# Kernel optimization log

Hardware: AMD Instinct MI355X
Metric: run time of the kernel (lower is better)

Reference implementation:

```python
import jax, jax.numpy as jnp
import numpy as np

N, C_S, C_Z, H, D = 512, 384, 128, 16, 24  # c_hidden per head
EPS = 1e-5

def _ln(x, g, b):
    m = jnp.mean(x, axis=-1, keepdims=True)
    v = jnp.mean(jnp.square(x - m), axis=-1, keepdims=True)
    return (x - m) * jax.lax.rsqrt(v + EPS) * g + b

def setup_inputs() -> dict:
    key = jax.random.key(0)
    ks = jax.random.split(key, 12)
    s = lambda fan: 1.0 / np.sqrt(fan)
    return {
        "a": jax.random.normal(ks[0], (1, N, C_S), jnp.float32),
        "z": jax.random.normal(ks[1], (1, N, N, C_Z), jnp.float32),
        "g_a": jnp.ones((C_S,), jnp.float32),
        "b_a": jnp.zeros((C_S,), jnp.float32),
        "g_z": jnp.ones((C_Z,), jnp.float32),
        "b_z": jnp.zeros((C_Z,), jnp.float32),
        "Wz": jax.random.normal(ks[2], (C_Z, H), jnp.float32) * s(C_Z),
        "bz": jnp.zeros((H,), jnp.float32),
        "Wq": jax.random.normal(ks[3], (C_S, H * D), jnp.float32) * s(C_S),
        "Wk": jax.random.normal(ks[4], (C_S, H * D), jnp.float32) * s(C_S),
        "Wv": jax.random.normal(ks[5], (C_S, H * D), jnp.float32) * s(C_S),
        "Wg": jax.random.normal(ks[6], (C_S, H * D), jnp.float32) * s(C_S),
        "bg": jnp.zeros((H * D,), jnp.float32),
        "Wo": jax.random.normal(ks[7], (H * D, C_S), jnp.float32) * s(H * D),
        "bo": jnp.zeros((C_S,), jnp.float32),
    }

def reference(a, z, g_a, b_a, g_z, b_z, Wz, bz, Wq, Wk, Wv, Wg, bg, Wo, bo):
    B = a.shape[0]
    a_n = _ln(a, g_a, b_a)                       # [B,N,C_S]
    z_n = _ln(z, g_z, b_z)                       # [B,N,N,C_Z]
    # linear_z then permute(0,3,1,2): [B,N,N,H] -> [B,H,N,N]
    pair_bias = jnp.einsum('bijc,ch->bhij', z_n, Wz) + bz[None, :, None, None]
    q = (a_n @ Wq).reshape(B, N, H, D) * (1.0 / np.sqrt(D))
    k = (a_n @ Wk).reshape(B, N, H, D)
    v = (a_n @ Wv).reshape(B, N, H, D)
    scores = jnp.einsum('bqhd,bkhd->bhqk', q, k) + pair_bias
    p = jax.nn.softmax(scores, axis=-1)
    o = jnp.einsum('bhqk,bkhd->bqhd', p, v)      # [B,N,H,D]
    g = jax.nn.sigmoid(a_n @ Wg + bg).reshape(B, N, H, D)
    o = (o * g).reshape(B, N, H * D)
    return o @ Wo + bo                            # [B,N,C_S]
```

## Files before the change

### kernel.cpp

```cpp
#include <hip/hip_runtime.h>
#include <math.h>

#define N 512
#define CS 384
#define CZ 128
#define NH 16
#define DH 24
#define HD 384
#define NN (N*N)
#define EPS 1e-5f

#define OFF_AN   0
#define OFF_QT   196608
#define OFF_KT   393216
#define OFF_VT   589824
#define OFF_GT   786432
#define OFF_OG   983040
#define OFF_WZ2  1179648
#define OFF_SH   1181696
#define OFF_BH   1181712
#define OFF_BIAS 1181728

__global__ void __launch_bounds__(256) ln_prep_kernel(const float* __restrict__ a, const float* __restrict__ g_a,
                                                      const float* __restrict__ b_a, float* __restrict__ an_out,
                                                      const float* __restrict__ g_z, const float* __restrict__ lnb_z,
                                                      const float* __restrict__ Wz, const float* __restrict__ bz,
                                                      float* __restrict__ wz2, float* __restrict__ sh,
                                                      float* __restrict__ bh) {
    __shared__ float ls[NH][17], lb[NH][17];
    __shared__ float l1[4], l2[4];
    const int t = threadIdx.x;
    if (blockIdx.x == 256) {
        for (int i = t; i < NH * CZ; i += 256) {
            int h = i >> 7, c = i & (CZ - 1);
            wz2[h * CZ + c] = g_z[c] * Wz[c * NH + h];
        }
        int h = t >> 4, seg = t & 15;
        float s = 0.f, b = 0.f;
        #pragma unroll
        for (int i = 0; i < 8; ++i) {
            int c = seg * 8 + i;
            float w = Wz[c * NH + h];
            s += g_z[c] * w;
            b += lnb_z[c] * w;
        }
        ls[h][seg] = s; lb[h][seg] = b;
        __syncthreads();
        if (t < NH) {
            float ss = 0.f, bb = 0.f;
            #pragma unroll
            for (int i = 0; i < 16; ++i) { ss += ls[t][i]; bb += lb[t][i]; }
            sh[t] = ss;
            bh[t] = bb + bz[t];
        }
        return;
    }
    const int half = t >> 7;
    const int tr = t & 127;
    const int r = blockIdx.x * 2 + half;
    const float* row = a + r * CS;
    float x0 = row[tr], x1 = row[tr + 128], x2 = row[tr + 256];
    float s1 = x0 + x1 + x2;
    float s2 = x0 * x0 + x1 * x1 + x2 * x2;
    #pragma unroll
    for (int m = 1; m < 64; m <<= 1) {
        s1 += __shfl_xor(s1, m, 64);
        s2 += __shfl_xor(s2, m, 64);
    }
    if ((t & 63) == 0) { l1[t >> 6] = s1; l2[t >> 6] = s2; }
    __syncthreads();
    s1 = l1[half * 2] + l1[half * 2 + 1];
    s2 = l2[half * 2] + l2[half * 2 + 1];
    float mu = s1 * (1.f / CS);
    float var = s2 * (1.f / CS) - mu * mu;
    float rs = rsqrtf(var + EPS);
    float* an = an_out + r * CS;
    an[tr]       = (x0 - mu) * rs * g_a[tr]       + b_a[tr];
    an[tr + 128] = (x1 - mu) * rs * g_a[tr + 128] + b_a[tr + 128];
    an[tr + 256] = (x2 - mu) * rs * g_a[tr + 256] + b_a[tr + 256];
}

__global__ void __launch_bounds__(256) qkvg_kernel(const float* __restrict__ Wq, const float* __restrict__ Wk,
                                                   const float* __restrict__ Wv, const float* __restrict__ Wg,
                                                   const float* __restrict__ bg, const float* __restrict__ an,
                                                   float* __restrict__ qt, float* __restrict__ kt,
                                                   float* __restrict__ vt, float* __restrict__ gt) {
    __shared__ float4 lan[64 * 8];
    const int t = threadIdx.x;
    const int lane = t & 63;
    const int w = __builtin_amdgcn_readfirstlane(t >> 6);
    const int s = blockIdx.x * 4 + w;
    const int n0 = s * 4;
    const int sel = n0 / HD;
    const int col = n0 - sel * HD;
    const float* Wm = (sel == 0) ? Wq : (sel == 1) ? Wk : (sel == 2) ? Wv : Wg;
    const int m0 = blockIdx.y * 64;
    const int m = m0 + lane;
    const float4* an4 = (const float4*)an;
    float acc[4];
    #pragma unroll
    for (int j = 0; j < 4; ++j) acc[j] = 0.f;
    for (int kb = 0; kb < CS; kb += 32) {
        __syncthreads();
        #pragma unroll
        for (int i = 0; i < 2; ++i) {
            const int idx = i * 256 + t;
            const int r = idx >> 3, c = idx & 7;
            lan[(r << 3) + (c ^ (r & 7))] = an4[(size_t)(m0 + r) * 96 + (kb >> 2) + c];
        }
        __syncthreads();
        float4 av[8];
        #pragma unroll
        for (int i = 0; i < 8; ++i) av[i] = lan[(lane << 3) + (i ^ (lane & 7))];
        #pragma unroll
        for (int i = 0; i < 8; ++i) {
            const float* wr = Wm + (kb + i * 4) * HD + col;
            #pragma unroll
            for (int j = 0; j < 4; ++j) {
                acc[j] += av[i].x * wr[j];
                acc[j] += av[i].y * wr[HD + j];
                acc[j] += av[i].z * wr[2 * HD + j];
                acc[j] += av[i].w * wr[3 * HD + j];
            }
        }
    }
    float* dst = (sel == 0) ? qt : (sel == 1) ? kt : (sel == 2) ? vt : gt;
    if (sel == 3) {
        #pragma unroll
        for (int j = 0; j < 4; ++j) acc[j] = 1.f / (1.f + __expf(-(acc[j] + bg[col + j])));
    } else if (sel == 0) {
        #pragma unroll
        for (int j = 0; j < 4; ++j) acc[j] *= 0.20412414523193153f;
    }
    const int h = col / DH, d0 = col - h * DH;
    float* dp = dst + (h * N + m) * DH + d0;
    #pragma unroll
    for (int j = 0; j < 4; ++j) dp[j] = acc[j];
}

__global__ void __launch_bounds__(256, 4) pairbias_kernel(const float* __restrict__ z,
                                                          const float* __restrict__ wz2,
                                                          const float* __restrict__ sh,
                                                          const float* __restrict__ bh,
                                                          float* __restrict__ bias) {
    __shared__ float4 lz[64 * 32];
    const int t = threadIdx.x;
    const int l = t & 63;
    const int w = __builtin_amdgcn_readfirstlane(t >> 6);
    const int h0 = w * 4;
    const int row0 = blockIdx.x * 64;

    const float4* zsrc = (const float4*)(z + (size_t)row0 * CZ);
    #pragma unroll
    for (int i = 0; i < 8; ++i) {
        const int g4 = i * 256 + t;
        float4 v = zsrc[g4];
        const int r = g4 >> 5, cc = g4 & 31;
        lz[r * 32 + (cc ^ (r & 31))] = v;
    }
    __syncthreads();

    const unsigned base = (unsigned)(l * 512 + ((l & 31) << 4));
    const char* lzb = (const char*)lz;
    float s1 = 0.f, s2 = 0.f;
    float dots[4];
    #pragma unroll
    for (int j = 0; j < 4; ++j) dots[j] = 0.f;
    #pragma unroll
    for (int cc = 0; cc < 32; ++cc) {
        float4 v = *(const float4*)(lzb + (base ^ (unsigned)(cc << 4)));
        s1 += v.x + v.y + v.z + v.w;
        s2 += v.x * v.x + v.y * v.y + v.z * v.z + v.w * v.w;
        #pragma unroll
        for (int j = 0; j < 4; ++j) {
            const float4 wv = ((const float4*)(wz2 + (h0 + j) * CZ))[cc];
            dots[j] += v.x * wv.x + v.y * wv.y + v.z * wv.z + v.w * wv.w;
        }
    }
    const float mu = s1 * (1.f / CZ);
    const float var = s2 * (1.f / CZ) - mu * mu;
    const float rr = rsqrtf(var + EPS);
    const int row = row0 + l;
    #pragma unroll
    for (int j = 0; j < 4; ++j)
        bias[(h0 + j) * NN + row] = rr * (dots[j] - mu * sh[h0 + j]) + bh[h0 + j];
}

__global__ void __launch_bounds__(256, 4) attn_kernel(const float* __restrict__ qt, const float* __restrict__ kt,
                                                      const float* __restrict__ vt, const float* __restrict__ gt,
                                                      const float* __restrict__ bias, float* __restrict__ og) {
    __shared__ float4 lzK[128 * 8];
    __shared__ float4 lzV[128 * 8];
    const int t = threadIdx.x;
    const int lane = t & 63;
    const int w = __builtin_amdgcn_readfirstlane(t >> 6);
    const int qhalf = lane >> 5;
    const int klane = lane & 31;
    const int h = blockIdx.y;
    const int q = blockIdx.x * 8 + w * 2 + qhalf;
    const float* qT = qt + h * N * DH;
    const float4* kT4 = (const float4*)(kt + h * N * DH);
    const float4* vT4 = (const float4*)(vt + h * N * DH);
    const float* brow = bias + h * NN + q * N;

    float qv[DH];
    #pragma unroll
    for (int d6 = 0; d6 < 6; ++d6) {
        float4 t4 = ((const float4*)(qT + q * DH))[d6];
        qv[d6 * 4 + 0] = t4.x; qv[d6 * 4 + 1] = t4.y; qv[d6 * 4 + 2] = t4.z; qv[d6 * 4 + 3] = t4.w;
    }
    float m_run = -1e30f, l_run = 0.f;
    float acc[DH];
    #pragma unroll
    for (int d = 0; d < DH; ++d) acc[d] = 0.f;

    for (int tile = 0; tile < 4; ++tile) {
        __syncthreads();
        const int kt0 = tile * 128;
        #pragma unroll
        for (int i = 0; i < 3; ++i) {
            const int idx = i * 256 + t;
            const int r = idx / 6, c = idx - r * 6;
            const int slot = (r << 3) + (c ^ (r & 7));
            lzK[slot] = kT4[kt0 * 6 + idx];
            lzV[slot] = vT4[kt0 * 6 + idx];
        }
        __syncthreads();
        float sc[4];
        #pragma unroll
        for (int j = 0; j < 4; ++j) {
            const int kk = j * 32 + klane;
            const float4* kr = lzK + (kk << 3);
            const int x = kk & 7;
            float4 k0 = kr[0 ^ x], k1 = kr[1 ^ x], k2 = kr[2 ^ x],
                   k3 = kr[3 ^ x], k4 = kr[4 ^ x], k5 = kr[5 ^ x];
            float s = qv[0]*k0.x + qv[1]*k0.y + qv[2]*k0.z + qv[3]*k0.w
                    + qv[4]*k1.x + qv[5]*k1.y + qv[6]*k1.z + qv[7]*k1.w
                    + qv[8]*k2.x + qv[9]*k2.y + qv[10]*k2.z + qv[11]*k2.w
                    + qv[12]*k3.x + qv[13]*k3.y + qv[14]*k3.z + qv[15]*k3.w
                    + qv[16]*k4.x + qv[17]*k4.y + qv[18]*k4.z + qv[19]*k4.w
                    + qv[20]*k5.x + qv[21]*k5.y + qv[22]*k5.z + qv[23]*k5.w;
            sc[j] = s + brow[kt0 + kk];
        }
        float tm = fmaxf(fmaxf(sc[0], sc[1]), fmaxf(sc[2], sc[3]));
        #pragma unroll
        for (int m = 1; m < 32; m <<= 1) tm = fmaxf(tm, __shfl_xor(tm, m, 64));
        const float m_new = fmaxf(m_run, tm);
        const float scale = __expf(m_run - m_new);
        l_run *= scale;
        #pragma unroll
        for (int d = 0; d < DH; ++d) acc[d] *= scale;
        float p[4], ps = 0.f;
        #pragma unroll
        for (int j = 0; j < 4; ++j) { p[j] = __expf(sc[j] - m_new); ps += p[j]; }
        #pragma unroll
        for (int m = 1; m < 32; m <<= 1) ps += __shfl_xor(ps, m, 64);
        l_run += ps;
        m_run = m_new;
        #pragma unroll
        for (int j = 0; j < 4; ++j) {
            const int kk = j * 32 + klane;
            const float4* vr = lzV + (kk << 3);
            const int x = kk & 7;
            float4 v0 = vr[0 ^ x], v1 = vr[1 ^ x], v2 = vr[2 ^ x],
                   v3 = vr[3 ^ x], v4 = vr[4 ^ x], v5 = vr[5 ^ x];
            const float pj = p[j];
            acc[0] += pj*v0.x;  acc[1] += pj*v0.y;  acc[2] += pj*v0.z;  acc[3] += pj*v0.w;
            acc[4] += pj*v1.x;  acc[5] += pj*v1.y;  acc[6] += pj*v1.z;  acc[7] += pj*v1.w;
            acc[8] += pj*v2.x;  acc[9] += pj*v2.y;  acc[10] += pj*v2.z; acc[11] += pj*v2.w;
            acc[12] += pj*v3.x; acc[13] += pj*v3.y; acc[14] += pj*v3.z; acc[15] += pj*v3.w;
            acc[16] += pj*v4.x; acc[17] += pj*v4.y; acc[18] += pj*v4.z; acc[19] += pj*v4.w;
            acc[20] += pj*v5.x; acc[21] += pj*v5.y; acc[22] += pj*v5.z; acc[23] += pj*v5.w;
        }
    }
    #pragma unroll
    for (int m = 1; m < 32; m <<= 1) {
        #pragma unroll
        for (int d = 0; d < DH; ++d) acc[d] += __shfl_xor(acc[d], m, 64);
    }
    const float inv = 1.f / l_run;
    float o = 0.f;
    #pragma unroll
    for (int d = 0; d < DH; ++d) o = (klane == d) ? acc[d] : o;
    if (klane < DH) {
        float g = gt[h * N * DH + q * DH + klane];
        og[q * HD + h * DH + klane] = o * inv * g;
    }
}

__global__ void __launch_bounds__(256) out_gemm_kernel(const float* __restrict__ Wo, const float* __restrict__ bo,
                                                       const float* __restrict__ og, float* __restrict__ out) {
    __shared__ float4 lo[64 * 8];
    const int t = threadIdx.x;
    const int lane = t & 63;
    const int w = __builtin_amdgcn_readfirstlane(t >> 6);
    const int s = blockIdx.x * 4 + w;
    const int c0 = s * 2;
    const int m0 = blockIdx.y * 64;
    const int m = m0 + lane;
    const float4* og4 = (const float4*)og;
    float acc[2];
    acc[0] = 0.f; acc[1] = 0.f;
    for (int kb = 0; kb < HD; kb += 32) {
        __syncthreads();
        #pragma unroll
        for (int i = 0; i < 2; ++i) {
            const int idx = i * 256 + t;
            const int r = idx >> 3, c = idx & 7;
            lo[(r << 3) + (c ^ (r & 7))] = og4[(size_t)(m0 + r) * 96 + (kb >> 2) + c];
        }
        __syncthreads();
        float4 av[8];
        #pragma unroll
        for (int i = 0; i < 8; ++i) av[i] = lo[(lane << 3) + (i ^ (lane & 7))];
        #pragma unroll
        for (int i = 0; i < 8; ++i) {
            const float* wr = Wo + (kb + i * 4) * CS + c0;
            #pragma unroll
            for (int j = 0; j < 2; ++j) {
                acc[j] += av[i].x * wr[j];
                acc[j] += av[i].y * wr[CS + j];
                acc[j] += av[i].z * wr[2 * CS + j];
                acc[j] += av[i].w * wr[3 * CS + j];
            }
        }
    }
    #pragma unroll
    for (int j = 0; j < 2; ++j) out[m * CS + c0 + j] = acc[j] + bo[c0 + j];
}

extern "C" void kernel_launch(void* const* d_in, const int* in_sizes, int n_in,
                              void* d_out, int out_size, void* d_ws, size_t ws_size,
                              hipStream_t stream) {
    const float* a    = (const float*)d_in[0];
    const float* z    = (const float*)d_in[1];
    const float* g_a  = (const float*)d_in[2];
    const float* b_a  = (const float*)d_in[3];
    const float* g_z  = (const float*)d_in[4];
    const float* b_z  = (const float*)d_in[5];
    const float* Wz   = (const float*)d_in[6];
    const float* bz   = (const float*)d_in[7];
    const float* Wq   = (const float*)d_in[8];
    const float* Wk   = (const float*)d_in[9];
    const float* Wv   = (const float*)d_in[10];
    const float* Wg   = (const float*)d_in[11];
    const float* bg   = (const float*)d_in[12];
    const float* Wo   = (const float*)d_in[13];
    const float* bo   = (const float*)d_in[14];
    float* ws  = (float*)d_ws;
    float* out = (float*)d_out;

    float* an   = ws + OFF_AN;
    float* qt   = ws + OFF_QT;
    float* kt   = ws + OFF_KT;
    float* vt   = ws + OFF_VT;
    float* gt   = ws + OFF_GT;
    float* ogp  = ws + OFF_OG;
    float* wz2  = ws + OFF_WZ2;
    float* shp  = ws + OFF_SH;
    float* bhp  = ws + OFF_BH;
    float* bias = ws + OFF_BIAS;

    hipLaunchKernelGGL(ln_prep_kernel, dim3(257),    dim3(256), 0, stream,
                       a, g_a, b_a, an, g_z, b_z, Wz, bz, wz2, shp, bhp);
    hipLaunchKernelGGL(qkvg_kernel,    dim3(96, 8),  dim3(256), 0, stream,
                       Wq, Wk, Wv, Wg, bg, an, qt, kt, vt, gt);
    hipLaunchKernelGGL(pairbias_kernel, dim3(4096),  dim3(256), 0, stream,
                       z, wz2, shp, bhp, bias);
    hipLaunchKernelGGL(attn_kernel,    dim3(64, 16), dim3(256), 0, stream,
                       qt, kt, vt, gt, bias, ogp);
    hipLaunchKernelGGL(out_gemm_kernel, dim3(48, 8), dim3(256), 0, stream,
                       Wo, bo, ogp, out);
}
```

Measured before the change: 333.8 us.

## Double-buffer z tiles in pair-bias kernel with register prefetch across four slices

Each pair-bias block now handles 256 rows in four 64-row slices instead of one. The next slice's z data is prefetched into registers while the current slice is computed from shared memory, using two LDS buffers. The goal is to hide global-load latency behind the LayerNorm and projection math on this memory-bound kernel. The cost is four times fewer blocks, double the LDS, more registers and lower occupancy (launch bounds drop from 4 to 2).

```diff
diff --git a/kernel.cpp b/kernel.cpp
--- a/kernel.cpp
+++ b/kernel.cpp
@@ -138,52 +138,67 @@
     for (int j = 0; j < 4; ++j) dp[j] = acc[j];
 }
 
-__global__ void __launch_bounds__(256, 4) pairbias_kernel(const float* __restrict__ z,
+__global__ void __launch_bounds__(256, 2) pairbias_kernel(const float* __restrict__ z,
                                                           const float* __restrict__ wz2,
                                                           const float* __restrict__ sh,
                                                           const float* __restrict__ bh,
                                                           float* __restrict__ bias) {
-    __shared__ float4 lz[64 * 32];
+    __shared__ float4 buf0[64 * 32];
+    __shared__ float4 buf1[64 * 32];
     const int t = threadIdx.x;
     const int l = t & 63;
     const int w = __builtin_amdgcn_readfirstlane(t >> 6);
     const int h0 = w * 4;
-    const int row0 = blockIdx.x * 64;
-
-    const float4* zsrc = (const float4*)(z + (size_t)row0 * CZ);
-    #pragma unroll
-    for (int i = 0; i < 8; ++i) {
-        const int g4 = i * 256 + t;
-        float4 v = zsrc[g4];
-        const int r = g4 >> 5, cc = g4 & 31;
-        lz[r * 32 + (cc ^ (r & 31))] = v;
-    }
-    __syncthreads();
-
-    const unsigned base = (unsigned)(l * 512 + ((l & 31) << 4));
-    const char* lzb = (const char*)lz;
-    float s1 = 0.f, s2 = 0.f;
-    float dots[4];
-    #pragma unroll
-    for (int j = 0; j < 4; ++j) dots[j] = 0.f;
-    #pragma unroll
-    for (int cc = 0; cc < 32; ++cc) {
-        float4 v = *(const float4*)(lzb + (base ^ (unsigned)(cc << 4)));
-        s1 += v.x + v.y + v.z + v.w;
-        s2 += v.x * v.x + v.y * v.y + v.z * v.z + v.w * v.w;
-        #pragma unroll
-        for (int j = 0; j < 4; ++j) {
-            const float4 wv = ((const float4*)(wz2 + (h0 + j) * CZ))[cc];
-            dots[j] += v.x * wv.x + v.y * wv.y + v.z * wv.z + v.w * wv.w;
-        }
-    }
-    const float mu = s1 * (1.f / CZ);
-    const float var = s2 * (1.f / CZ) - mu * mu;
-    const float rr = rsqrtf(var + EPS);
-    const int row = row0 + l;
-    #pragma unroll
-    for (int j = 0; j < 4; ++j)
-        bias[(h0 + j) * NN + row] = rr * (dots[j] - mu * sh[h0 + j]) + bh[h0 + j];
+    const int row0 = blockIdx.x * 256;
+    const float4* zsrc = (const float4*)z + (size_t)row0 * 32;
+
+#define PB_LOAD(s, rr) { const float4* p_ = zsrc + (s) * 2048; \
+    _Pragma("unroll") for (int i = 0; i < 8; ++i) rr[i] = p_[i * 256 + t]; }
+
+#define PB_WRITE(rr, bufp) { _Pragma("unroll") for (int i = 0; i < 8; ++i) { \
+    const int g4_ = i * 256 + t; const int r_ = g4_ >> 5, cc_ = g4_ & 31; \
+    bufp[r_ * 32 + (cc_ ^ (r_ & 31))] = rr[i]; } }
+
+#define PB_COMPUTE(s, bufp) { \
+    const char* lzb_ = (const char*)bufp; \
+    const unsigned base_ = (unsigned)(l * 512 + ((l & 31) << 4)); \
+    float s1_ = 0.f, s2_ = 0.f, d0_ = 0.f, d1_ = 0.f, d2_ = 0.f, d3_ = 0.f; \
+    _Pragma("unroll") for (int cc = 0; cc < 32; ++cc) { \
+        float4 v_ = *(const float4*)(lzb_ + (base_ ^ (unsigned)(cc << 4))); \
+        s1_ += v_.x + v_.y + v_.z + v_.w; \
+        s2_ += v_.x * v_.x + v_.y * v_.y + v_.z * v_.z + v_.w * v_.w; \
+        const float4 w0_ = ((const float4*)(wz2 + (h0 + 0) * CZ))[cc]; \
+        const float4 w1_ = ((const float4*)(wz2 + (h0 + 1) * CZ))[cc]; \
+        const float4 w2_ = ((const float4*)(wz2 + (h0 + 2) * CZ))[cc]; \
+        const float4 w3_ = ((const float4*)(wz2 + (h0 + 3) * CZ))[cc]; \
+        d0_ += v_.x * w0_.x + v_.y * w0_.y + v_.z * w0_.z + v_.w * w0_.w; \
+        d1_ += v_.x * w1_.x + v_.y * w1_.y + v_.z * w1_.z + v_.w * w1_.w; \
+        d2_ += v_.x * w2_.x + v_.y * w2_.y + v_.z * w2_.z + v_.w * w2_.w; \
+        d3_ += v_.x * w3_.x + v_.y * w3_.y + v_.z * w3_.z + v_.w * w3_.w; } \
+    const float mu_ = s1_ * (1.f / CZ); \
+    const float var_ = s2_ * (1.f / CZ) - mu_ * mu_; \
+    const float rs_ = rsqrtf(var_ + EPS); \
+    const int row_ = row0 + (s) * 64 + l; \
+    bias[(h0 + 0) * NN + row_] = rs_ * (d0_ - mu_ * sh[h0 + 0]) + bh[h0 + 0]; \
+    bias[(h0 + 1) * NN + row_] = rs_ * (d1_ - mu_ * sh[h0 + 1]) + bh[h0 + 1]; \
+    bias[(h0 + 2) * NN + row_] = rs_ * (d2_ - mu_ * sh[h0 + 2]) + bh[h0 + 2]; \
+    bias[(h0 + 3) * NN + row_] = rs_ * (d3_ - mu_ * sh[h0 + 3]) + bh[h0 + 3]; }
+
+    float4 ra[8], rb[8];
+    PB_LOAD(0, ra); PB_WRITE(ra, buf0); __syncthreads();
+    PB_LOAD(1, rb);
+    PB_COMPUTE(0, buf0);
+    PB_WRITE(rb, buf1); __syncthreads();
+    PB_LOAD(2, ra);
+    PB_COMPUTE(1, buf1);
+    PB_WRITE(ra, buf0); __syncthreads();
+    PB_LOAD(3, rb);
+    PB_COMPUTE(2, buf0);
+    PB_WRITE(rb, buf1); __syncthreads();
+    PB_COMPUTE(3, buf1);
+#undef PB_LOAD
+#undef PB_WRITE
+#undef PB_COMPUTE
 }
 
 __global__ void __launch_bounds__(256, 4) attn_kernel(const float* __restrict__ qt, const float* __restrict__ kt,
@@ -365,7 +380,7 @@
                        a, g_a, b_a, an, g_z, b_z, Wz, bz, wz2, shp, bhp);
     hipLaunchKernelGGL(qkvg_kernel,    dim3(96, 8),  dim3(256), 0, stream,
                        Wq, Wk, Wv, Wg, bg, an, qt, kt, vt, gt);
-    hipLaunchKernelGGL(pairbias_kernel, dim3(4096),  dim3(256), 0, stream,
+    hipLaunchKernelGGL(pairbias_kernel, dim3(1024),  dim3(256), 0, stream,
                        z, wz2, shp, bhp, bias);
     hipLaunchKernelGGL(attn_kernel,    dim3(64, 16), dim3(256), 0, stream,
                        qt, kt, vt, gt, bias, ogp);
```

Result: slower. 399.5 us (+19.7%).

## Restructure pair-bias kernel so each thread owns a z row and computes all heads

Applied to the files above, without the earlier changes.

In the pair-bias kernel each block now stages 256 rows of z (128 KB of LDS) instead of 64. Each thread handles one row across all 16 heads, rather than one wave per 4 heads re-reading the same row. This removes the 4x redundant LDS reads and layernorm statistics per row. Global loads are issued as two register batches to overlap fetching with LDS writes. The trade-off is much higher LDS and register use, which limits the kernel to one block per CU and reduces latency hiding for the memory-bound z stream.

```diff
diff --git a/kernel.cpp b/kernel.cpp
--- a/kernel.cpp
+++ b/kernel.cpp
@@ -138,52 +138,61 @@
     for (int j = 0; j < 4; ++j) dp[j] = acc[j];
 }
 
-__global__ void __launch_bounds__(256, 4) pairbias_kernel(const float* __restrict__ z,
+__global__ void __launch_bounds__(256, 1) pairbias_kernel(const float* __restrict__ z,
                                                           const float* __restrict__ wz2,
                                                           const float* __restrict__ sh,
                                                           const float* __restrict__ bh,
                                                           float* __restrict__ bias) {
-    __shared__ float4 lz[64 * 32];
-    const int t = threadIdx.x;
-    const int l = t & 63;
-    const int w = __builtin_amdgcn_readfirstlane(t >> 6);
-    const int h0 = w * 4;
-    const int row0 = blockIdx.x * 64;
-
-    const float4* zsrc = (const float4*)(z + (size_t)row0 * CZ);
-    #pragma unroll
-    for (int i = 0; i < 8; ++i) {
-        const int g4 = i * 256 + t;
-        float4 v = zsrc[g4];
-        const int r = g4 >> 5, cc = g4 & 31;
-        lz[r * 32 + (cc ^ (r & 31))] = v;
-    }
+    __shared__ float4 lz[256 * 32];
+    const int t = threadIdx.x;
+    const int row0 = blockIdx.x * 256;
+    const float4* zsrc = (const float4*)z + (size_t)row0 * 32;
+
+#define PB_WR(rr, b) { _Pragma("unroll") for (int i = 0; i < 8; ++i) { \
+    const int g4_ = ((b) * 8 + i) * 256 + t; \
+    const int r_ = g4_ >> 5, cc_ = g4_ & 31; \
+    lz[r_ * 32 + (cc_ ^ (r_ & 31))] = rr[i]; } }
+
+    float4 ra[8], rb[8];
+    #pragma unroll
+    for (int i = 0; i < 8; ++i) ra[i] = zsrc[(0 * 8 + i) * 256 + t];
+    #pragma unroll
+    for (int i = 0; i < 8; ++i) rb[i] = zsrc[(1 * 8 + i) * 256 + t];
+    PB_WR(ra, 0);
+    #pragma unroll
+    for (int i = 0; i < 8; ++i) ra[i] = zsrc[(2 * 8 + i) * 256 + t];
+    PB_WR(rb, 1);
+    #pragma unroll
+    for (int i = 0; i < 8; ++i) rb[i] = zsrc[(3 * 8 + i) * 256 + t];
+    PB_WR(ra, 2);
+    PB_WR(rb, 3);
+#undef PB_WR
     __syncthreads();
 
-    const unsigned base = (unsigned)(l * 512 + ((l & 31) << 4));
     const char* lzb = (const char*)lz;
+    const unsigned base = (unsigned)(t * 512 + ((t & 31) << 4));
     float s1 = 0.f, s2 = 0.f;
-    float dots[4];
-    #pragma unroll
-    for (int j = 0; j < 4; ++j) dots[j] = 0.f;
-    #pragma unroll
+    float d[16];
+    #pragma unroll
+    for (int j = 0; j < 16; ++j) d[j] = 0.f;
+    #pragma unroll 4
     for (int cc = 0; cc < 32; ++cc) {
         float4 v = *(const float4*)(lzb + (base ^ (unsigned)(cc << 4)));
         s1 += v.x + v.y + v.z + v.w;
         s2 += v.x * v.x + v.y * v.y + v.z * v.z + v.w * v.w;
         #pragma unroll
-        for (int j = 0; j < 4; ++j) {
-            const float4 wv = ((const float4*)(wz2 + (h0 + j) * CZ))[cc];
-            dots[j] += v.x * wv.x + v.y * wv.y + v.z * wv.z + v.w * wv.w;
+        for (int j = 0; j < 16; ++j) {
+            const float4 wv = ((const float4*)(wz2 + j * CZ))[cc];
+            d[j] += v.x * wv.x + v.y * wv.y + v.z * wv.z + v.w * wv.w;
         }
     }
     const float mu = s1 * (1.f / CZ);
     const float var = s2 * (1.f / CZ) - mu * mu;
-    const float rr = rsqrtf(var + EPS);
-    const int row = row0 + l;
-    #pragma unroll
-    for (int j = 0; j < 4; ++j)
-        bias[(h0 + j) * NN + row] = rr * (dots[j] - mu * sh[h0 + j]) + bh[h0 + j];
+    const float rs = rsqrtf(var + EPS);
+    const int row = row0 + t;
+    #pragma unroll
+    for (int j = 0; j < 16; ++j)
+        bias[j * NN + row] = rs * (d[j] - mu * sh[j]) + bh[j];
 }
 
 __global__ void __launch_bounds__(256, 4) attn_kernel(const float* __restrict__ qt, const float* __restrict__ kt,
@@ -365,7 +374,7 @@
                        a, g_a, b_a, an, g_z, b_z, Wz, bz, wz2, shp, bhp);
     hipLaunchKernelGGL(qkvg_kernel,    dim3(96, 8),  dim3(256), 0, stream,
                        Wq, Wk, Wv, Wg, bg, an, qt, kt, vt, gt);
-    hipLaunchKernelGGL(pairbias_kernel, dim3(4096),  dim3(256), 0, stream,
+    hipLaunchKernelGGL(pairbias_kernel, dim3(1024),  dim3(256), 0, stream,
                        z, wz2, shp, bhp, bias);
     hipLaunchKernelGGL(attn_kernel,    dim3(64, 16), dim3(256), 0, stream,
                        qt, kt, vt, gt, bias, ogp);
```

Measured after the change: 418.4 us. 1.25x slower.
